# Kernel tuning notes

Hardware: AMD Instinct MI355X
Metric: run time of the kernel (lower is better)

## Reference

```python
import jax, jax.numpy as jnp
import numpy as np

N_NODES = 100000
N_EDGES = 800000
IN_DIM, HID_DIM, OUT_DIM = 128, 256, 40


def setup_inputs() -> dict:
    key = jax.random.key(0)
    ks = jax.random.split(key, 8)
    x = jax.random.normal(ks[0], (N_NODES, IN_DIM), dtype=jnp.float32)
    edge_index = jax.random.randint(ks[1], (2, N_EDGES), 0, N_NODES, dtype=jnp.int64)
    # PyG SAGEConv params: lin_l (neighbor path, with bias), lin_r (root path, no bias)
    def glorot(k, fan_in, fan_out):
        lim = np.sqrt(6.0 / (fan_in + fan_out)).astype(np.float32)
        return jax.random.uniform(k, (fan_in, fan_out), jnp.float32, -lim, lim)
    W1l = glorot(ks[2], IN_DIM, HID_DIM)
    W1r = glorot(ks[3], IN_DIM, HID_DIM)
    b1 = jnp.zeros((HID_DIM,), jnp.float32)
    W2l = glorot(ks[4], HID_DIM, OUT_DIM)
    W2r = glorot(ks[5], HID_DIM, OUT_DIM)
    b2 = jnp.zeros((OUT_DIM,), jnp.float32)
    return {"x": x, "edge_index": edge_index, "W1l": W1l, "b1": b1, "W1r": W1r,
            "W2l": W2l, "b2": b2, "W2r": W2r}


def _sage_conv(x, src, dst, Wl, b, Wr, n_nodes):
    # mean aggregation of neighbor features: gather x[src], scatter-add to dst, divide by degree
    msg = x[src]                                              # [E, D]
    agg = jax.ops.segment_sum(msg, dst, num_segments=n_nodes)  # [N, D]
    cnt = jax.ops.segment_sum(jnp.ones((src.shape[0],), x.dtype), dst,
                              num_segments=n_nodes)            # [N]
    agg = agg / jnp.maximum(cnt, 1.0)[:, None]
    # out = lin_l(mean_agg) + lin_r(x)  (lin_l carries the bias in PyG)
    return agg @ Wl + b + x @ Wr


def reference(x, edge_index, W1l, b1, W1r, W2l, b2, W2r):
    src, dst = edge_index[0], edge_index[1]
    n = x.shape[0]
    h = _sage_conv(x, src, dst, W1l, b1, W1r, n)
    h = jax.nn.relu(h)
    # F.dropout(training=self.training): identity at inference
    out = _sage_conv(h, src, dst, W2l, b2, W2r, n)
    return out
```

## Files before the change

### kernel.cpp

```cpp
#include <hip/hip_runtime.h>
#include <hip/hip_bf16.h>


#define NN   100000
#define NNP  100096
#define NE   800000
#define NB1  391

typedef unsigned short ushortT;
typedef __attribute__((ext_vector_type(8))) short bf16x8;
typedef __attribute__((ext_vector_type(4))) float f32x4;

__device__ __forceinline__ unsigned short f2b(float f) {
    unsigned u = __float_as_uint(f);
    return (unsigned short)((u + 0x7fffu + ((u >> 16) & 1u)) >> 16);
}
__device__ __forceinline__ float b2f(unsigned short v) {
    return __uint_as_float(((unsigned)v) << 16);
}
__device__ __forceinline__ void llds16(const unsigned short* g, unsigned short* s) {
    __builtin_amdgcn_global_load_lds(
        (const __attribute__((address_space(1))) void*)g,
        (__attribute__((address_space(3))) void*)s, 16, 0, 0);
}

__global__ __launch_bounds__(256) void k_prep_rank(
        const float* __restrict__ x,
        const float* __restrict__ W1l, const float* __restrict__ W1r,
        const float* __restrict__ W2l, const float* __restrict__ W2r,
        ushortT* __restrict__ Ac, ushortT* __restrict__ WT1,
        ushortT* __restrict__ WT2,
        const int* __restrict__ dst, int* __restrict__ deg,
        int* __restrict__ rank) {
    int bid = blockIdx.x;
    if (bid < 12500) {
        int t = bid * 256 + threadIdx.x;
        int row = t >> 5, c4 = t & 31;
        float4 v = *(const float4*)&x[(size_t)row * 128 + c4 * 4];
        ushortT* p = Ac + (size_t)row * 256 + 128 + c4 * 4;
        p[0] = f2b(v.x); p[1] = f2b(v.y); p[2] = f2b(v.z); p[3] = f2b(v.w);

        if (t < 65536) {
            int n = t >> 8, k = t & 255;
            float w = (k < 128) ? W1l[(size_t)k * 256 + n]
                                : W1r[(size_t)(k - 128) * 256 + n];
            WT1[t] = f2b(w);
        } else if (t < 65536 + 20480) {
            int j = t - 65536;
            int n = j >> 8, k = j & 255;
            float w = (n < 40) ? W2l[(size_t)k * 40 + n]
                               : W2r[(size_t)k * 40 + (n - 40)];
            WT2[j] = f2b(w);
        }
    } else {
        int e = (bid - 12500) * 256 + threadIdx.x;
        if (e < NE) rank[e] = atomicAdd(&deg[dst[e]], 1);
    }
}

__global__ __launch_bounds__(256) void k_scan1(const int* __restrict__ deg,
                                               int* __restrict__ rp,
                                               int* __restrict__ bsum) {
    __shared__ int s[256];
    int t = threadIdx.x;
    int i = blockIdx.x * 256 + t;
    int v = (i < NN) ? deg[i] : 0;
    s[t] = v;
    __syncthreads();
    for (int off = 1; off < 256; off <<= 1) {
        int add = (t >= off) ? s[t - off] : 0;
        __syncthreads();
        s[t] += add;
        __syncthreads();
    }
    if (i < NN) rp[i] = s[t] - v;
    if (t == 255) bsum[blockIdx.x] = s[255];
}

__global__ __launch_bounds__(512) void k_scan2(int* __restrict__ bsum) {
    __shared__ int s[512];
    int t = threadIdx.x;
    int v = (t < NB1) ? bsum[t] : 0;
    s[t] = v;
    __syncthreads();
    for (int off = 1; off < 512; off <<= 1) {
        int add = (t >= off) ? s[t - off] : 0;
        __syncthreads();
        s[t] += add;
        __syncthreads();
    }
    if (t < NB1) bsum[t] = s[t] - v;
}

__global__ __launch_bounds__(256) void k_scan3(int* __restrict__ rp,
                                               const int* __restrict__ bsum) {
    int i = blockIdx.x * 256 + threadIdx.x;
    if (i < NN) rp[i] += bsum[blockIdx.x];
    if (i == 0) rp[NN] = NE;
}

__global__ __launch_bounds__(256) void k_fill(const int* __restrict__ src,
                                              const int* __restrict__ dst,
                                              const int* __restrict__ rank,
                                              const int* __restrict__ rp,
                                              int* __restrict__ col) {
    int e = blockIdx.x * 256 + threadIdx.x;
    if (e < NE) col[rp[dst[e]] + rank[e]] = src[e];
}

__global__ __launch_bounds__(256) void k_agg1(const int* __restrict__ rp,
                                              const int* __restrict__ col,
                                              ushortT* __restrict__ Ac) {
    int node = blockIdx.x * 4 + (threadIdx.x >> 6);
    int l = threadIdx.x & 63;
    if (node >= NN) return;
    int seg = l >> 4, dl = l & 15;
    int beg = rp[node];
    int deg = rp[node + 1] - beg;
    float a[8] = {0.f, 0.f, 0.f, 0.f, 0.f, 0.f, 0.f, 0.f};
    for (int base = 0; base < deg; base += 64) {
        int cnt = min(64, deg - base);
        int cv = col[beg + base + min(l, cnt - 1)];
        for (int j = 0; j < cnt; j += 8) {
            int e0 = j + seg, e1 = j + 4 + seg;
            int i0 = __shfl(cv, min(e0, cnt - 1));
            int i1 = __shfl(cv, min(e1, cnt - 1));
            bf16x8 v0 = {0, 0, 0, 0, 0, 0, 0, 0};
            bf16x8 v1 = {0, 0, 0, 0, 0, 0, 0, 0};
            if (e0 < cnt) v0 = *(const bf16x8*)(Ac + (size_t)i0 * 256 + 128 + dl * 8);
            if (e1 < cnt) v1 = *(const bf16x8*)(Ac + (size_t)i1 * 256 + 128 + dl * 8);
#pragma unroll
            for (int i = 0; i < 8; ++i)
                a[i] += b2f((unsigned short)v0[i]) + b2f((unsigned short)v1[i]);
        }
    }
#pragma unroll
    for (int i = 0; i < 8; ++i) {
        a[i] += __shfl_xor(a[i], 16);
        a[i] += __shfl_xor(a[i], 32);
    }
    if (seg == 0) {
        float inv = 1.0f / fmaxf((float)deg, 1.0f);
        bf16x8 o;
#pragma unroll
        for (int i = 0; i < 8; ++i) o[i] = (short)f2b(a[i] * inv);
        *(bf16x8*)(Ac + (size_t)node * 256 + dl * 8) = o;
    }
}

#define HSP 264
__global__ __launch_bounds__(256, 3) void k_fused(
        const ushortT* __restrict__ Ac, const ushortT* __restrict__ WT1,
        const float* __restrict__ b1, const ushortT* __restrict__ WT2,
        const float* __restrict__ b2, ushortT* __restrict__ y2,
        float* __restrict__ t) {
    __shared__ ushortT As[64 * 64];
    __shared__ ushortT Bs[64 * HSP];
    const int tid = threadIdx.x, l = tid & 63, wid = tid >> 6;
    const int m0 = blockIdx.x * 64;
    const int q = l >> 4, r = l & 15;
    const int swz = (l & 7) ^ ((l >> 3) & 7);

    f32x4 acc[4][4];
#pragma unroll
    for (int i = 0; i < 4; ++i)
#pragma unroll
        for (int j = 0; j < 4; ++j) acc[i][j] = (f32x4){0.f, 0.f, 0.f, 0.f};

    for (int kt = 0; kt < 256; kt += 64) {
#pragma unroll
        for (int i = 0; i < 2; ++i) {
            int flat = wid * 2 + i;
            int row = flat * 8 + (l >> 3);
            llds16(Ac + (size_t)(m0 + row) * 256 + kt + swz * 8, &As[flat * 512]);
        }
#pragma unroll
        for (int i = 0; i < 8; ++i) {
            int flat = wid * 8 + i;
            int row = flat * 8 + (l >> 3);
            llds16(WT1 + (size_t)row * 256 + kt + swz * 8, &Bs[flat * 512]);
        }
        __syncthreads();
#pragma unroll
        for (int ks = 0; ks < 64; ks += 32) {
            bf16x8 af[4], bfr[4];
            const int cs = (((ks >> 3) + q) ^ (r & 7)) * 8;
#pragma unroll
            for (int mt = 0; mt < 4; ++mt)
                af[mt] = *(const bf16x8*)&As[(mt * 16 + r) * 64 + cs];
#pragma unroll
            for (int nt = 0; nt < 4; ++nt)
                bfr[nt] = *(const bf16x8*)&Bs[(wid * 64 + nt * 16 + r) * 64 + cs];
#pragma unroll
            for (int mt = 0; mt < 4; ++mt)
#pragma unroll
                for (int nt = 0; nt < 4; ++nt)
                    acc[mt][nt] = __builtin_amdgcn_mfma_f32_16x16x32_bf16(
                        af[mt], bfr[nt], acc[mt][nt], 0, 0, 0);
        }
        __syncthreads();
    }
#pragma unroll
    for (int nt = 0; nt < 4; ++nt) {
        int colb = wid * 64 + nt * 16 + r;
        float bb = b1[colb];
#pragma unroll
        for (int mt = 0; mt < 4; ++mt) {
            int rowb = mt * 16 + q * 4;
#pragma unroll
            for (int j = 0; j < 4; ++j)
                Bs[(rowb + j) * HSP + colb] = f2b(fmaxf(acc[mt][nt][j] + bb, 0.f));
        }
    }
    __syncthreads();

    f32x4 acc2[2][4];
#pragma unroll
    for (int i = 0; i < 2; ++i)
#pragma unroll
        for (int j = 0; j < 4; ++j) acc2[i][j] = (f32x4){0.f, 0.f, 0.f, 0.f};
#pragma unroll
    for (int kk = 0; kk < 256; kk += 32) {
        bf16x8 af[4];
#pragma unroll
        for (int mt = 0; mt < 4; ++mt)
            af[mt] = *(const bf16x8*)&Bs[(mt * 16 + r) * HSP + kk + q * 8];
#pragma unroll
        for (int cc = 0; cc < 2; ++cc) {
            int ct = wid + cc * 4;
            if (ct < 5) {
                bf16x8 bq = *(const bf16x8*)(WT2 + (size_t)(ct * 16 + r) * 256 + kk + q * 8);
#pragma unroll
                for (int mt = 0; mt < 4; ++mt)
                    acc2[cc][mt] = __builtin_amdgcn_mfma_f32_16x16x32_bf16(
                        af[mt], bq, acc2[cc][mt], 0, 0, 0);
            }
        }
    }
#pragma unroll
    for (int cc = 0; cc < 2; ++cc) {
        int ct = wid + cc * 4;
        if (ct >= 5) continue;
        int c = ct * 16 + r;
        float bb = (c >= 40) ? b2[c - 40] : 0.f;
#pragma unroll
        for (int mt = 0; mt < 4; ++mt) {
            int row0 = m0 + mt * 16 + q * 4;
#pragma unroll
            for (int j = 0; j < 4; ++j) {
                float v = acc2[cc][mt][j];
                if (c < 40)
                    y2[(size_t)(row0 + j) * 40 + c] = f2b(v);
                else
                    t[(size_t)(row0 + j) * 40 + (c - 40)] = v + bb;
            }
        }
    }
}

__global__ __launch_bounds__(256) void k_agg2(const int* __restrict__ rp,
                                              const int* __restrict__ col,
                                              const ushortT* __restrict__ y2,
                                              const float* __restrict__ t,
                                              float* __restrict__ out) {
    int node = blockIdx.x * 4 + (threadIdx.x >> 6);
    int l = threadIdx.x & 63;
    if (node >= NN) return;
    int seg = l >> 4, dl = l & 15;
    int beg = rp[node];
    int deg = rp[node + 1] - beg;
    bool act = dl < 10;
    float a0 = 0.f, a1 = 0.f, a2 = 0.f, a3 = 0.f;
    for (int base = 0; base < deg; base += 64) {
        int cnt = min(64, deg - base);
        int cv = col[beg + base + min(l, cnt - 1)];
        for (int j = 0; j < cnt; j += 8) {
            int e0 = j + seg, e1 = j + 4 + seg;
            int i0 = __shfl(cv, min(e0, cnt - 1));
            int i1 = __shfl(cv, min(e1, cnt - 1));
            ushort4 v0 = {0, 0, 0, 0}, v1 = {0, 0, 0, 0};
            if (e0 < cnt && act) v0 = *(const ushort4*)(y2 + (size_t)i0 * 40 + dl * 4);
            if (e1 < cnt && act) v1 = *(const ushort4*)(y2 + (size_t)i1 * 40 + dl * 4);
            a0 += b2f(v0.x) + b2f(v1.x);
            a1 += b2f(v0.y) + b2f(v1.y);
            a2 += b2f(v0.z) + b2f(v1.z);
            a3 += b2f(v0.w) + b2f(v1.w);
        }
    }
    a0 += __shfl_xor(a0, 16); a0 += __shfl_xor(a0, 32);
    a1 += __shfl_xor(a1, 16); a1 += __shfl_xor(a1, 32);
    a2 += __shfl_xor(a2, 16); a2 += __shfl_xor(a2, 32);
    a3 += __shfl_xor(a3, 16); a3 += __shfl_xor(a3, 32);
    if (seg == 0 && act) {
        float inv = 1.0f / fmaxf((float)deg, 1.0f);
        size_t o = (size_t)node * 40 + dl * 4;
        float4 tv = *(const float4*)&t[o];
        float4 ov;
        ov.x = a0 * inv + tv.x;
        ov.y = a1 * inv + tv.y;
        ov.z = a2 * inv + tv.z;
        ov.w = a3 * inv + tv.w;
        *(float4*)&out[o] = ov;
    }
}

extern "C" void kernel_launch(void* const* d_in, const int* in_sizes, int n_in,
                              void* d_out, int out_size, void* d_ws, size_t ws_size,
                              hipStream_t stream) {
    const float* x   = (const float*)d_in[0];
    const int*   ei  = (const int*)d_in[1];
    const int*   src = ei;
    const int*   dst = ei + NE;
    const float* W1l = (const float*)d_in[2];
    const float* b1  = (const float*)d_in[3];
    const float* W1r = (const float*)d_in[4];
    const float* W2l = (const float*)d_in[5];
    const float* b2  = (const float*)d_in[6];
    const float* W2r = (const float*)d_in[7];
    float* out = (float*)d_out;

    size_t off = 0;
    char* base = (char*)d_ws;
    auto alloc = [&](size_t bytes) -> void* {
        void* p = base + off;
        off += (bytes + 255) & ~(size_t)255;
        return p;
    };
    int*     deg   = (int*)alloc((size_t)NN * 4);
    int*     rp    = (int*)alloc((size_t)(NN + 1) * 4);
    int*     rank  = (int*)alloc((size_t)NE * 4);
    int*     col   = (int*)alloc((size_t)NE * 4);
    int*     bsum  = (int*)alloc(512 * 4);
    ushortT* Ac    = (ushortT*)alloc((size_t)NNP * 256 * 2);
    ushortT* y2    = (ushortT*)alloc((size_t)NNP * 40 * 2);
    float*   t     = (float*)alloc((size_t)NNP * 40 * 4);
    ushortT* WT1   = (ushortT*)alloc(256 * 256 * 2);
    ushortT* WT2   = (ushortT*)alloc(80 * 256 * 2);

    hipMemsetAsync(deg, 0, (size_t)NN * 4, stream);
    k_prep_rank<<<15625, 256, 0, stream>>>(x, W1l, W1r, W2l, W2r, Ac, WT1, WT2,
                                           dst, deg, rank);
    k_scan1<<<NB1, 256, 0, stream>>>(deg, rp, bsum);
    k_scan2<<<1, 512, 0, stream>>>(bsum);
    k_scan3<<<NB1, 256, 0, stream>>>(rp, bsum);
    k_fill<<<(NE + 255) / 256, 256, 0, stream>>>(src, dst, rank, rp, col);
    k_agg1<<<(NN + 3) / 4, 256, 0, stream>>>(rp, col, Ac);
    k_fused<<<NNP / 64, 256, 0, stream>>>(Ac, WT1, b1, WT2, b2, y2, t);
    k_agg2<<<(NN + 3) / 4, 256, 0, stream>>>(rp, col, y2, t, out);
}
```

Baseline: 276.6 us.

## Privatize degree counters, drop scan3, range-partition CSR fill, store root term in bf16

Degree counting now spreads atomics over 8 private counter copies chosen by block index, which is meant to cut atomic contention. The scan emits per-copy prefix offsets, and the separate block-offset pass is removed by adding bsum lazily in fill, agg1 and agg2. k_fill is range-partitioned by destination so that each block writes col within a node range, to improve write locality at the cost of reading dst eight times. The root-path term t is stored in bf16 instead of fp32 to halve its traffic, which loses some precision.

```diff
diff --git a/kernel.cpp b/kernel.cpp
--- a/kernel.cpp
+++ b/kernel.cpp
@@ -30,7 +30,7 @@
         const float* __restrict__ W2l, const float* __restrict__ W2r,
         ushortT* __restrict__ Ac, ushortT* __restrict__ WT1,
         ushortT* __restrict__ WT2,
-        const int* __restrict__ dst, int* __restrict__ deg,
+        const int* __restrict__ dst, int* __restrict__ deg8,
         int* __restrict__ rank) {
     int bid = blockIdx.x;
     if (bid < 12500) {
@@ -53,18 +53,27 @@
             WT2[j] = f2b(w);
         }
     } else {
-        int e = (bid - 12500) * 256 + threadIdx.x;
-        if (e < NE) rank[e] = atomicAdd(&deg[dst[e]], 1);
-    }
-}
-
-__global__ __launch_bounds__(256) void k_scan1(const int* __restrict__ deg,
+        int idx = bid - 12500;
+        int e = idx * 256 + threadIdx.x;
+        int r = idx & 7;
+        rank[e] = atomicAdd(&deg8[r * NN + dst[e]], 1);
+    }
+}
+
+__global__ __launch_bounds__(256) void k_scan1(const int* __restrict__ deg8,
                                                int* __restrict__ rp,
+                                               int* __restrict__ rpp,
                                                int* __restrict__ bsum) {
     __shared__ int s[256];
     int t = threadIdx.x;
     int i = blockIdx.x * 256 + t;
-    int v = (i < NN) ? deg[i] : 0;
+    int d8[8];
+    int v = 0;
+#pragma unroll
+    for (int r = 0; r < 8; ++r) {
+        d8[r] = (i < NN) ? deg8[r * NN + i] : 0;
+        v += d8[r];
+    }
     s[t] = v;
     __syncthreads();
     for (int off = 1; off < 256; off <<= 1) {
@@ -73,7 +82,16 @@
         s[t] += add;
         __syncthreads();
     }
-    if (i < NN) rp[i] = s[t] - v;
+    int ex = s[t] - v;
+    if (i <= NN) rp[i] = ex;
+    if (i < NN) {
+        int run = ex;
+#pragma unroll
+        for (int r = 0; r < 8; ++r) {
+            rpp[r * NN + i] = run;
+            run += d8[r];
+        }
+    }
     if (t == 255) bsum[blockIdx.x] = s[255];
 }
 
@@ -92,31 +110,40 @@
     if (t < NB1) bsum[t] = s[t] - v;
 }
 
-__global__ __launch_bounds__(256) void k_scan3(int* __restrict__ rp,
-                                               const int* __restrict__ bsum) {
-    int i = blockIdx.x * 256 + threadIdx.x;
-    if (i < NN) rp[i] += bsum[blockIdx.x];
-    if (i == 0) rp[NN] = NE;
-}
-
 __global__ __launch_bounds__(256) void k_fill(const int* __restrict__ src,
                                               const int* __restrict__ dst,
                                               const int* __restrict__ rank,
-                                              const int* __restrict__ rp,
+                                              const int* __restrict__ rpp,
+                                              const int* __restrict__ bsum,
                                               int* __restrict__ col) {
-    int e = blockIdx.x * 256 + threadIdx.x;
-    if (e < NE) col[rp[dst[e]] + rank[e]] = src[e];
+    int fbid = blockIdx.x;
+    int chunk = fbid >> 3;
+    int lo = (fbid & 7) * 12500, hi = lo + 12500;
+    int base = chunk * 2048 + threadIdx.x;
+#pragma unroll
+    for (int j = 0; j < 8; ++j) {
+        int e = base + j * 256;
+        if (e < NE) {
+            int d = dst[e];
+            if (d >= lo && d < hi) {
+                int r = (e >> 8) & 7;
+                col[bsum[d >> 8] + rpp[r * NN + d] + rank[e]] = src[e];
+            }
+        }
+    }
 }
 
 __global__ __launch_bounds__(256) void k_agg1(const int* __restrict__ rp,
+                                              const int* __restrict__ bsum,
                                               const int* __restrict__ col,
                                               ushortT* __restrict__ Ac) {
     int node = blockIdx.x * 4 + (threadIdx.x >> 6);
     int l = threadIdx.x & 63;
     if (node >= NN) return;
     int seg = l >> 4, dl = l & 15;
-    int beg = rp[node];
-    int deg = rp[node + 1] - beg;
+    int beg = rp[node] + bsum[node >> 8];
+    int end = rp[node + 1] + bsum[(node + 1) >> 8];
+    int deg = end - beg;
     float a[8] = {0.f, 0.f, 0.f, 0.f, 0.f, 0.f, 0.f, 0.f};
     for (int base = 0; base < deg; base += 64) {
         int cnt = min(64, deg - base);
@@ -153,7 +180,7 @@
         const ushortT* __restrict__ Ac, const ushortT* __restrict__ WT1,
         const float* __restrict__ b1, const ushortT* __restrict__ WT2,
         const float* __restrict__ b2, ushortT* __restrict__ y2,
-        float* __restrict__ t) {
+        ushortT* __restrict__ t) {
     __shared__ ushortT As[64 * 64];
     __shared__ ushortT Bs[64 * HSP];
     const int tid = threadIdx.x, l = tid & 63, wid = tid >> 6;
@@ -252,23 +279,25 @@
                 if (c < 40)
                     y2[(size_t)(row0 + j) * 40 + c] = f2b(v);
                 else
-                    t[(size_t)(row0 + j) * 40 + (c - 40)] = v + bb;
+                    t[(size_t)(row0 + j) * 40 + (c - 40)] = f2b(v + bb);
             }
         }
     }
 }
 
 __global__ __launch_bounds__(256) void k_agg2(const int* __restrict__ rp,
+                                              const int* __restrict__ bsum,
                                               const int* __restrict__ col,
                                               const ushortT* __restrict__ y2,
-                                              const float* __restrict__ t,
+                                              const ushortT* __restrict__ t,
                                               float* __restrict__ out) {
     int node = blockIdx.x * 4 + (threadIdx.x >> 6);
     int l = threadIdx.x & 63;
     if (node >= NN) return;
     int seg = l >> 4, dl = l & 15;
-    int beg = rp[node];
-    int deg = rp[node + 1] - beg;
+    int beg = rp[node] + bsum[node >> 8];
+    int end = rp[node + 1] + bsum[(node + 1) >> 8];
+    int deg = end - beg;
     bool act = dl < 10;
     float a0 = 0.f, a1 = 0.f, a2 = 0.f, a3 = 0.f;
     for (int base = 0; base < deg; base += 64) {
@@ -294,12 +323,12 @@
     if (seg == 0 && act) {
         float inv = 1.0f / fmaxf((float)deg, 1.0f);
         size_t o = (size_t)node * 40 + dl * 4;
-        float4 tv = *(const float4*)&t[o];
+        ushort4 tv = *(const ushort4*)&t[o];
         float4 ov;
-        ov.x = a0 * inv + tv.x;
-        ov.y = a1 * inv + tv.y;
-        ov.z = a2 * inv + tv.z;
-        ov.w = a3 * inv + tv.w;
+        ov.x = a0 * inv + b2f(tv.x);
+        ov.y = a1 * inv + b2f(tv.y);
+        ov.z = a2 * inv + b2f(tv.z);
+        ov.w = a3 * inv + b2f(tv.w);
         *(float4*)&out[o] = ov;
     }
 }
@@ -326,25 +355,25 @@
         off += (bytes + 255) & ~(size_t)255;
         return p;
     };
-    int*     deg   = (int*)alloc((size_t)NN * 4);
+    int*     deg8  = (int*)alloc((size_t)8 * NN * 4);
     int*     rp    = (int*)alloc((size_t)(NN + 1) * 4);
+    int*     rpp   = (int*)alloc((size_t)8 * NN * 4);
     int*     rank  = (int*)alloc((size_t)NE * 4);
     int*     col   = (int*)alloc((size_t)NE * 4);
     int*     bsum  = (int*)alloc(512 * 4);
     ushortT* Ac    = (ushortT*)alloc((size_t)NNP * 256 * 2);
     ushortT* y2    = (ushortT*)alloc((size_t)NNP * 40 * 2);
-    float*   t     = (float*)alloc((size_t)NNP * 40 * 4);
+    ushortT* t     = (ushortT*)alloc((size_t)NNP * 40 * 2);
     ushortT* WT1   = (ushortT*)alloc(256 * 256 * 2);
     ushortT* WT2   = (ushortT*)alloc(80 * 256 * 2);
 
-    hipMemsetAsync(deg, 0, (size_t)NN * 4, stream);
+    hipMemsetAsync(deg8, 0, (size_t)8 * NN * 4, stream);
     k_prep_rank<<<15625, 256, 0, stream>>>(x, W1l, W1r, W2l, W2r, Ac, WT1, WT2,
-                                           dst, deg, rank);
-    k_scan1<<<NB1, 256, 0, stream>>>(deg, rp, bsum);
+                                           dst, deg8, rank);
+    k_scan1<<<NB1, 256, 0, stream>>>(deg8, rp, rpp, bsum);
     k_scan2<<<1, 512, 0, stream>>>(bsum);
-    k_scan3<<<NB1, 256, 0, stream>>>(rp, bsum);
-    k_fill<<<(NE + 255) / 256, 256, 0, stream>>>(src, dst, rank, rp, col);
-    k_agg1<<<(NN + 3) / 4, 256, 0, stream>>>(rp, col, Ac);
+    k_fill<<<391 * 8, 256, 0, stream>>>(src, dst, rank, rpp, bsum, col);
+    k_agg1<<<(NN + 3) / 4, 256, 0, stream>>>(rp, bsum, col, Ac);
     k_fused<<<NNP / 64, 256, 0, stream>>>(Ac, WT1, b1, WT2, b2, y2, t);
-    k_agg2<<<(NN + 3) / 4, 256, 0, stream>>>(rp, col, y2, t, out);
-}
+    k_agg2<<<(NN + 3) / 4, 256, 0, stream>>>(rp, bsum, col, y2, t, out);
+}
```

Result: no change. 271.7 us (-1.8%).
